# Performance work log

Hardware: AMD Instinct MI355X
Metric: run time of the kernel (lower is better)

Reference implementation:

```python
import jax, jax.numpy as jnp
import numpy as np

H = 32        # num_attention_heads
KVH = 8       # num_key_value_heads
D = 2048      # hidden_size
HD = D // H   # head_dim = 64
GROUPS = H // KVH


def setup_inputs() -> dict:
    key = jax.random.key(0)
    k1, k2, k3, k4 = jax.random.split(key, 4)
    B, T = 2, 2048
    x = jax.random.normal(k1, (B, T, D), dtype=jnp.float32)
    wq = jax.random.normal(k2, (D, H * HD), dtype=jnp.float32) * (D ** -0.5)
    wkv = jax.random.normal(k3, (D, 2 * KVH * HD), dtype=jnp.float32) * (D ** -0.5)
    wo = jax.random.normal(k4, (H * HD, D), dtype=jnp.float32) * (D ** -0.5)
    return {"x": x, "wq": wq, "wkv": wkv, "wo": wo}


def reference(x, wq, wkv, wo):
    B, T, _ = x.shape
    scale = HD ** -0.5
    # projections
    q = (x @ wq).reshape(B, T, H, HD).transpose(0, 2, 1, 3)        # [B,H,T,hd]
    kv = x @ wkv                                                    # [B,T,2*KVH*hd]
    k, v = jnp.split(kv, 2, axis=-1)
    k = k.reshape(B, T, KVH, HD).transpose(0, 2, 1, 3)              # [B,KVH,T,hd]
    v = v.reshape(B, T, KVH, HD).transpose(0, 2, 1, 3)
    # repeat_interleave KV heads to match Q heads
    k = jnp.repeat(k, GROUPS, axis=1)                               # [B,H,T,hd]
    v = jnp.repeat(v, GROUPS, axis=1)
    scores = jnp.einsum('bhqd,bhkd->bhqk', q, k) * scale            # [B,H,T,T]
    causal = jnp.triu(jnp.ones((T, T), dtype=bool), k=1)
    scores = jnp.where(causal, -jnp.inf, scores)
    attn = jax.nn.softmax(scores, axis=-1)
    out = jnp.einsum('bhqk,bhkd->bhqd', attn, v)                    # [B,H,T,hd]
    out = out.transpose(0, 2, 1, 3).reshape(B, T, H * HD)
    return out @ wo
```

## Files before the change

kernel.cpp:

```cpp
#include <hip/hip_runtime.h>

using bf16   = __bf16;
using bf16x8 = __attribute__((ext_vector_type(8))) __bf16;
using f32x4  = __attribute__((ext_vector_type(4))) float;

#define T_SEQ 2048
#define NQKV 3072

__device__ __forceinline__ void async_cp16(const bf16* g, bf16* l) {
  __builtin_amdgcn_global_load_lds((__attribute__((address_space(1))) void*)(void*)g,
                                   (__attribute__((address_space(3))) void*)l, 16, 0, 0);
}

__global__ __launch_bounds__(256) void cvt_kernel(const float* __restrict__ in,
                                                  bf16* __restrict__ out) {
  long i = ((long)blockIdx.x * 256 + threadIdx.x) * 8;
  float4 a = *(const float4*)(in + i);
  float4 c = *(const float4*)(in + i + 4);
  bf16x8 v;
  v[0] = (bf16)a.x; v[1] = (bf16)a.y; v[2] = (bf16)a.z; v[3] = (bf16)a.w;
  v[4] = (bf16)c.x; v[5] = (bf16)c.y; v[6] = (bf16)c.z; v[7] = (bf16)c.w;
  *(bf16x8*)(out + i) = v;
}

__global__ __launch_bounds__(256) void transpose_cvt(const float* __restrict__ in,
                                                     bf16* __restrict__ out,
                                                     int R, int C) {
  __shared__ float tile[32][33];
  const int tc = blockIdx.x * 32;
  const int tr = blockIdx.y * 32;
  const int t = threadIdx.x;
  const int lr = t >> 5;
  const int lc = t & 31;
#pragma unroll
  for (int i = 0; i < 4; ++i)
    tile[lr + i * 8][lc] = in[(size_t)(tr + lr + i * 8) * C + tc + lc];
  __syncthreads();
#pragma unroll
  for (int i = 0; i < 4; ++i)
    out[(size_t)(tc + lr + i * 8) * R + tr + lc] = (bf16)tile[lc][lr + i * 8];
}

__global__ __launch_bounds__(256) void transpose_v(const bf16* __restrict__ in,
                                                   bf16* __restrict__ out) {
  __shared__ bf16 tile[32][33];
  const int c0 = blockIdx.x * 32;
  const int r0 = blockIdx.y * 32;
  const int t = threadIdx.x;
  const int lr = t >> 5;
  const int lc = t & 31;
#pragma unroll
  for (int i = 0; i < 4; ++i)
    tile[lr + i * 8][lc] = in[(size_t)(r0 + lr + i * 8) * NQKV + 2560 + c0 + lc];
  __syncthreads();
#pragma unroll
  for (int i = 0; i < 4; ++i) {
    int c = c0 + lr + i * 8;
    int r = r0 + lc;
    out[(size_t)((r >> 11) * 512 + c) * 2048 + (r & 2047)] = tile[lc][lr + i * 8];
  }
}

template <bool OUT_BF16>
__global__ __launch_bounds__(256, 3)
void gemm_kernel(const bf16* __restrict__ A, const bf16* __restrict__ Bt,
                 void* __restrict__ Cout, int Kdim, int Ndim) {
  __shared__ __attribute__((aligned(16))) bf16 As[128 * 64];
  __shared__ __attribute__((aligned(16))) bf16 Bs[128 * 64];
  const int tid  = threadIdx.x;
  const int lane = tid & 63;
  const int wave = tid >> 6;
  const int l16  = lane & 15;
  const int q4   = lane >> 4;
  const long m0 = (long)blockIdx.y * 128;
  const long n0 = (long)blockIdx.x * 128;
  const int wm = (wave >> 1) * 64;
  const int wn = (wave & 1) * 64;

  f32x4 acc[4][4] = {};

  for (int k0 = 0; k0 < Kdim; k0 += 64) {
    __syncthreads();
#pragma unroll
    for (int rr = 0; rr < 4; ++rr) {
      int ci  = rr * 256 + tid;
      int row = ci >> 3;
      int chp = ci & 7;
      int ch  = chp ^ (row & 7);
      async_cp16(A + (m0 + row) * (long)Kdim + k0 + ch * 8, &As[ci * 8]);
      async_cp16(Bt + (n0 + row) * (long)Kdim + k0 + ch * 8, &Bs[ci * 8]);
    }
    __syncthreads();
#pragma unroll
    for (int ks = 0; ks < 2; ++ks) {
      bf16x8 af[4], bfr[4];
#pragma unroll
      for (int mt = 0; mt < 4; ++mt) {
        int row = wm + mt * 16 + l16;
        int chp = (ks * 4 + q4) ^ (row & 7);
        af[mt] = *(const bf16x8*)&As[row * 64 + chp * 8];
      }
#pragma unroll
      for (int nt = 0; nt < 4; ++nt) {
        int row = wn + nt * 16 + l16;
        int chp = (ks * 4 + q4) ^ (row & 7);
        bfr[nt] = *(const bf16x8*)&Bs[row * 64 + chp * 8];
      }
#pragma unroll
      for (int mt = 0; mt < 4; ++mt)
#pragma unroll
        for (int nt = 0; nt < 4; ++nt)
          acc[mt][nt] = __builtin_amdgcn_mfma_f32_16x16x32_bf16(af[mt], bfr[nt],
                                                                acc[mt][nt], 0, 0, 0);
    }
  }
#pragma unroll
  for (int mt = 0; mt < 4; ++mt)
#pragma unroll
    for (int nt = 0; nt < 4; ++nt)
#pragma unroll
      for (int r = 0; r < 4; ++r) {
        long row = m0 + wm + mt * 16 + q4 * 4 + r;
        long col = n0 + wn + nt * 16 + l16;
        float v = acc[mt][nt][r];
        if constexpr (OUT_BF16)
          ((bf16*)Cout)[row * Ndim + col] = (bf16)v;
        else
          ((float*)Cout)[row * Ndim + col] = v;
      }
}

__global__ __launch_bounds__(256, 3)
void attn_kernel(const bf16* __restrict__ qkv, const bf16* __restrict__ vT,
                 bf16* __restrict__ outb) {
  __shared__ __attribute__((aligned(16))) bf16 Ks[64 * 72];
  __shared__ __attribute__((aligned(16))) bf16 Vs[64 * 72];
  __shared__ __attribute__((aligned(16))) bf16 Ps[4][32 * 72];

  const int tid  = threadIdx.x;
  const int lane = tid & 63;
  const int wave = tid >> 6;
  const int l16  = lane & 15;
  const int q4   = lane >> 4;

  const int bid = blockIdx.x;
  const int qt  = 15 - (bid >> 6);
  const int bh  = bid & 63;
  const int b   = bh >> 5;
  const int h   = bh & 31;
  const int kvh = h >> 2;
  const long rowbase = (long)b * T_SEQ;

  const int qrow0 = qt * 128;
  const int wq0   = qrow0 + wave * 32;
  const float cexp = 0.125f * 1.4426950408889634f;

  bf16x8 aq[2][2];
#pragma unroll
  for (int mt = 0; mt < 2; ++mt)
#pragma unroll
    for (int ks = 0; ks < 2; ++ks)
      aq[mt][ks] = *(const bf16x8*)(qkv +
          (rowbase + wq0 + mt * 16 + l16) * (long)NQKV + h * 64 + ks * 32 + q4 * 8);

  bf16x8 ones_f;
#pragma unroll
  for (int i = 0; i < 8; ++i) ones_f[i] = (l16 == 0) ? (bf16)1.0f : (bf16)0.0f;

  f32x4 o[2][4] = {};
  f32x4 o_l[2] = {};

  for (int j0 = 0; j0 < qrow0 + 128; j0 += 64) {
    __syncthreads();
    {
      int r  = tid >> 2;
      int c0 = (tid & 3) * 16;
      const bf16* srcK = qkv + (rowbase + j0 + r) * (long)NQKV + 2048 + kvh * 64 + c0;
      *(bf16x8*)&Ks[r * 72 + c0]     = *(const bf16x8*)srcK;
      *(bf16x8*)&Ks[r * 72 + c0 + 8] = *(const bf16x8*)(srcK + 8);
      const bf16* srcV = vT + ((long)b * 512 + kvh * 64 + r) * 2048 + j0 + c0;
      *(bf16x8*)&Vs[r * 72 + c0]     = *(const bf16x8*)srcV;
      *(bf16x8*)&Vs[r * 72 + c0 + 8] = *(const bf16x8*)(srcV + 8);
    }
    __syncthreads();
    if (j0 > wq0 + 31) continue;

    f32x4 s[2][4] = {};
#pragma unroll
    for (int ks = 0; ks < 2; ++ks) {
      bf16x8 bk[4];
#pragma unroll
      for (int nt = 0; nt < 4; ++nt)
        bk[nt] = *(const bf16x8*)&Ks[(nt * 16 + l16) * 72 + ks * 32 + q4 * 8];
#pragma unroll
      for (int mt = 0; mt < 2; ++mt)
#pragma unroll
        for (int nt = 0; nt < 4; ++nt)
          s[mt][nt] = __builtin_amdgcn_mfma_f32_16x16x32_bf16(aq[mt][ks], bk[nt],
                                                              s[mt][nt], 0, 0, 0);
    }

    if (j0 + 63 > wq0) {
#pragma unroll
      for (int mt = 0; mt < 2; ++mt)
#pragma unroll
        for (int nt = 0; nt < 4; ++nt)
#pragma unroll
          for (int r = 0; r < 4; ++r) {
            int rg = wq0 + mt * 16 + q4 * 4 + r;
            int cg = j0 + nt * 16 + l16;
            if (cg > rg) s[mt][nt][r] = -__builtin_inff();
          }
    }

#pragma unroll
    for (int mt = 0; mt < 2; ++mt)
#pragma unroll
      for (int nt = 0; nt < 4; ++nt)
#pragma unroll
        for (int r = 0; r < 4; ++r) {
          float pv = exp2f(s[mt][nt][r] * cexp);
          Ps[wave][(mt * 16 + q4 * 4 + r) * 72 + nt * 16 + l16] = (bf16)pv;
        }

#pragma unroll
    for (int ks = 0; ks < 2; ++ks) {
      bf16x8 ap[2], bv[4];
#pragma unroll
      for (int mt = 0; mt < 2; ++mt)
        ap[mt] = *(const bf16x8*)&Ps[wave][(mt * 16 + l16) * 72 + ks * 32 + q4 * 8];
#pragma unroll
      for (int dt = 0; dt < 4; ++dt)
        bv[dt] = *(const bf16x8*)&Vs[(dt * 16 + l16) * 72 + ks * 32 + q4 * 8];
#pragma unroll
      for (int mt = 0; mt < 2; ++mt) {
#pragma unroll
        for (int dt = 0; dt < 4; ++dt)
          o[mt][dt] = __builtin_amdgcn_mfma_f32_16x16x32_bf16(ap[mt], bv[dt],
                                                              o[mt][dt], 0, 0, 0);
        o_l[mt] = __builtin_amdgcn_mfma_f32_16x16x32_bf16(ap[mt], ones_f,
                                                          o_l[mt], 0, 0, 0);
      }
    }
  }

#pragma unroll
  for (int mt = 0; mt < 2; ++mt) {
    float inv[4];
#pragma unroll
    for (int r = 0; r < 4; ++r) {
      float lsum = __shfl(o_l[mt][r], lane & 48);
      inv[r] = 1.0f / lsum;
    }
#pragma unroll
    for (int dt = 0; dt < 4; ++dt)
#pragma unroll
      for (int r = 0; r < 4; ++r) {
        long row = rowbase + qrow0 + wave * 32 + mt * 16 + q4 * 4 + r;
        int col = h * 64 + dt * 16 + l16;
        outb[row * 2048 + col] = (bf16)(o[mt][dt][r] * inv[r]);
      }
  }
}

extern "C" void kernel_launch(void* const* d_in, const int* in_sizes, int n_in,
                              void* d_out, int out_size, void* d_ws, size_t ws_size,
                              hipStream_t stream) {
  const float* x   = (const float*)d_in[0];
  const float* wq  = (const float*)d_in[1];
  const float* wkv = (const float*)d_in[2];
  const float* wo  = (const float*)d_in[3];
  float* out = (float*)d_out;
  char* ws = (char*)d_ws;

  bf16* xbf  = (bf16*)(ws + 0);
  bf16* w1   = (bf16*)(ws + 16777216);
  bf16* qkv  = (bf16*)(ws + 29360128);
  bf16* attn = xbf;
  bf16* vT   = w1;

  const size_t need_parallel = 54525952u + 8388608u;
  bf16* woT;
  bool woT_early;
  if (ws_size >= need_parallel) {
    woT = (bf16*)(ws + 54525952);
    woT_early = true;
  } else {
    woT = qkv;
    woT_early = false;
  }

  cvt_kernel<<<4096, 256, 0, stream>>>(x, xbf);
  transpose_cvt<<<dim3(64, 64), 256, 0, stream>>>(wq, w1, 2048, 2048);
  transpose_cvt<<<dim3(32, 64), 256, 0, stream>>>(wkv, w1 + 2048L * 2048, 2048, 1024);
  if (woT_early)
    transpose_cvt<<<dim3(64, 64), 256, 0, stream>>>(wo, woT, 2048, 2048);

  gemm_kernel<true><<<dim3(24, 32), 256, 0, stream>>>(xbf, w1, (void*)qkv, 2048, 3072);

  transpose_v<<<dim3(16, 128), 256, 0, stream>>>(qkv, vT);

  attn_kernel<<<1024, 256, 0, stream>>>(qkv, vT, attn);

  if (!woT_early)
    transpose_cvt<<<dim3(64, 64), 256, 0, stream>>>(wo, woT, 2048, 2048);

  gemm_kernel<false><<<dim3(16, 32), 256, 0, stream>>>(attn, woT, (void*)out, 2048, 2048);
}
```

Before: 279.4 us.

## Use 64-row query tiles with paired causal tiles per block for load balance

The attention kernel now processes 64-row query tiles (16 rows per wave) and each block handles two tiles, qt and 31-qt, so every block does roughly the same amount of causal work. This halves per-wave accumulator registers and the P staging buffer, and raises the occupancy hint from 3 to 4 blocks per CU. In exchange, each K/V tile loaded into LDS feeds only 16 query rows per wave, so reuse of the staged data per load drops.

```diff
diff --git a/kernel.cpp b/kernel.cpp
--- a/kernel.cpp
+++ b/kernel.cpp
@@ -130,12 +130,12 @@
       }
 }
 
-__global__ __launch_bounds__(256, 3)
+__global__ __launch_bounds__(256, 4)
 void attn_kernel(const bf16* __restrict__ qkv, const bf16* __restrict__ vT,
                  bf16* __restrict__ outb) {
   __shared__ __attribute__((aligned(16))) bf16 Ks[64 * 72];
   __shared__ __attribute__((aligned(16))) bf16 Vs[64 * 72];
-  __shared__ __attribute__((aligned(16))) bf16 Ps[4][32 * 72];
+  __shared__ __attribute__((aligned(16))) bf16 Ps[4][16 * 72];
 
   const int tid  = threadIdx.x;
   const int lane = tid & 63;
@@ -144,121 +144,107 @@
   const int q4   = lane >> 4;
 
   const int bid = blockIdx.x;
-  const int qt  = 15 - (bid >> 6);
+  const int pairi = bid >> 6;
   const int bh  = bid & 63;
   const int b   = bh >> 5;
   const int h   = bh & 31;
   const int kvh = h >> 2;
   const long rowbase = (long)b * T_SEQ;
-
-  const int qrow0 = qt * 128;
-  const int wq0   = qrow0 + wave * 32;
   const float cexp = 0.125f * 1.4426950408889634f;
 
-  bf16x8 aq[2][2];
-#pragma unroll
-  for (int mt = 0; mt < 2; ++mt)
+  bf16x8 ones_f;
+#pragma unroll
+  for (int i = 0; i < 8; ++i) ones_f[i] = (l16 == 0) ? (bf16)1.0f : (bf16)0.0f;
+
+#pragma unroll
+  for (int ph = 0; ph < 2; ++ph) {
+    const int qt    = ph ? (31 - pairi) : pairi;
+    const int qrow0 = qt * 64;
+    const int wq0   = qrow0 + wave * 16;
+
+    bf16x8 aq[2];
 #pragma unroll
     for (int ks = 0; ks < 2; ++ks)
-      aq[mt][ks] = *(const bf16x8*)(qkv +
-          (rowbase + wq0 + mt * 16 + l16) * (long)NQKV + h * 64 + ks * 32 + q4 * 8);
-
-  bf16x8 ones_f;
-#pragma unroll
-  for (int i = 0; i < 8; ++i) ones_f[i] = (l16 == 0) ? (bf16)1.0f : (bf16)0.0f;
-
-  f32x4 o[2][4] = {};
-  f32x4 o_l[2] = {};
-
-  for (int j0 = 0; j0 < qrow0 + 128; j0 += 64) {
-    __syncthreads();
-    {
-      int r  = tid >> 2;
-      int c0 = (tid & 3) * 16;
-      const bf16* srcK = qkv + (rowbase + j0 + r) * (long)NQKV + 2048 + kvh * 64 + c0;
-      *(bf16x8*)&Ks[r * 72 + c0]     = *(const bf16x8*)srcK;
-      *(bf16x8*)&Ks[r * 72 + c0 + 8] = *(const bf16x8*)(srcK + 8);
-      const bf16* srcV = vT + ((long)b * 512 + kvh * 64 + r) * 2048 + j0 + c0;
-      *(bf16x8*)&Vs[r * 72 + c0]     = *(const bf16x8*)srcV;
-      *(bf16x8*)&Vs[r * 72 + c0 + 8] = *(const bf16x8*)(srcV + 8);
-    }
-    __syncthreads();
-    if (j0 > wq0 + 31) continue;
-
-    f32x4 s[2][4] = {};
-#pragma unroll
-    for (int ks = 0; ks < 2; ++ks) {
-      bf16x8 bk[4];
+      aq[ks] = *(const bf16x8*)(qkv +
+          (rowbase + wq0 + l16) * (long)NQKV + h * 64 + ks * 32 + q4 * 8);
+
+    f32x4 o[4] = {};
+    f32x4 o_l = {};
+
+    for (int j0 = 0; j0 <= qrow0; j0 += 64) {
+      __syncthreads();
+      {
+        int r  = tid >> 2;
+        int c0 = (tid & 3) * 16;
+        const bf16* srcK = qkv + (rowbase + j0 + r) * (long)NQKV + 2048 + kvh * 64 + c0;
+        *(bf16x8*)&Ks[r * 72 + c0]     = *(const bf16x8*)srcK;
+        *(bf16x8*)&Ks[r * 72 + c0 + 8] = *(const bf16x8*)(srcK + 8);
+        const bf16* srcV = vT + ((long)b * 512 + kvh * 64 + r) * 2048 + j0 + c0;
+        *(bf16x8*)&Vs[r * 72 + c0]     = *(const bf16x8*)srcV;
+        *(bf16x8*)&Vs[r * 72 + c0 + 8] = *(const bf16x8*)(srcV + 8);
+      }
+      __syncthreads();
+      if (j0 > wq0 + 15) continue;
+
+      f32x4 s[4] = {};
+#pragma unroll
+      for (int ks = 0; ks < 2; ++ks) {
+        bf16x8 bk[4];
+#pragma unroll
+        for (int nt = 0; nt < 4; ++nt)
+          bk[nt] = *(const bf16x8*)&Ks[(nt * 16 + l16) * 72 + ks * 32 + q4 * 8];
+#pragma unroll
+        for (int nt = 0; nt < 4; ++nt)
+          s[nt] = __builtin_amdgcn_mfma_f32_16x16x32_bf16(aq[ks], bk[nt],
+                                                          s[nt], 0, 0, 0);
+      }
+
+      if (j0 + 63 > wq0) {
+#pragma unroll
+        for (int nt = 0; nt < 4; ++nt)
+#pragma unroll
+          for (int r = 0; r < 4; ++r) {
+            int rg = wq0 + q4 * 4 + r;
+            int cg = j0 + nt * 16 + l16;
+            if (cg > rg) s[nt][r] = -__builtin_inff();
+          }
+      }
+
 #pragma unroll
       for (int nt = 0; nt < 4; ++nt)
-        bk[nt] = *(const bf16x8*)&Ks[(nt * 16 + l16) * 72 + ks * 32 + q4 * 8];
-#pragma unroll
-      for (int mt = 0; mt < 2; ++mt)
-#pragma unroll
-        for (int nt = 0; nt < 4; ++nt)
-          s[mt][nt] = __builtin_amdgcn_mfma_f32_16x16x32_bf16(aq[mt][ks], bk[nt],
-                                                              s[mt][nt], 0, 0, 0);
-    }
-
-    if (j0 + 63 > wq0) {
-#pragma unroll
-      for (int mt = 0; mt < 2; ++mt)
-#pragma unroll
-        for (int nt = 0; nt < 4; ++nt)
-#pragma unroll
-          for (int r = 0; r < 4; ++r) {
-            int rg = wq0 + mt * 16 + q4 * 4 + r;
-            int cg = j0 + nt * 16 + l16;
-            if (cg > rg) s[mt][nt][r] = -__builtin_inff();
-          }
-    }
-
-#pragma unroll
-    for (int mt = 0; mt < 2; ++mt)
-#pragma unroll
-      for (int nt = 0; nt < 4; ++nt)
 #pragma unroll
         for (int r = 0; r < 4; ++r) {
-          float pv = exp2f(s[mt][nt][r] * cexp);
-          Ps[wave][(mt * 16 + q4 * 4 + r) * 72 + nt * 16 + l16] = (bf16)pv;
+          float pv = exp2f(s[nt][r] * cexp);
+          Ps[wave][(q4 * 4 + r) * 72 + nt * 16 + l16] = (bf16)pv;
         }
 
 #pragma unroll
-    for (int ks = 0; ks < 2; ++ks) {
-      bf16x8 ap[2], bv[4];
-#pragma unroll
-      for (int mt = 0; mt < 2; ++mt)
-        ap[mt] = *(const bf16x8*)&Ps[wave][(mt * 16 + l16) * 72 + ks * 32 + q4 * 8];
-#pragma unroll
-      for (int dt = 0; dt < 4; ++dt)
-        bv[dt] = *(const bf16x8*)&Vs[(dt * 16 + l16) * 72 + ks * 32 + q4 * 8];
-#pragma unroll
-      for (int mt = 0; mt < 2; ++mt) {
+      for (int ks = 0; ks < 2; ++ks) {
+        bf16x8 ap = *(const bf16x8*)&Ps[wave][l16 * 72 + ks * 32 + q4 * 8];
+        bf16x8 bv[4];
 #pragma unroll
         for (int dt = 0; dt < 4; ++dt)
-          o[mt][dt] = __builtin_amdgcn_mfma_f32_16x16x32_bf16(ap[mt], bv[dt],
-                                                              o[mt][dt], 0, 0, 0);
-        o_l[mt] = __builtin_amdgcn_mfma_f32_16x16x32_bf16(ap[mt], ones_f,
-                                                          o_l[mt], 0, 0, 0);
-      }
-    }
-  }
-
-#pragma unroll
-  for (int mt = 0; mt < 2; ++mt) {
+          bv[dt] = *(const bf16x8*)&Vs[(dt * 16 + l16) * 72 + ks * 32 + q4 * 8];
+#pragma unroll
+        for (int dt = 0; dt < 4; ++dt)
+          o[dt] = __builtin_amdgcn_mfma_f32_16x16x32_bf16(ap, bv[dt], o[dt], 0, 0, 0);
+        o_l = __builtin_amdgcn_mfma_f32_16x16x32_bf16(ap, ones_f, o_l, 0, 0, 0);
+      }
+    }
+
     float inv[4];
 #pragma unroll
     for (int r = 0; r < 4; ++r) {
-      float lsum = __shfl(o_l[mt][r], lane & 48);
+      float lsum = __shfl(o_l[r], lane & 48);
       inv[r] = 1.0f / lsum;
     }
 #pragma unroll
     for (int dt = 0; dt < 4; ++dt)
 #pragma unroll
       for (int r = 0; r < 4; ++r) {
-        long row = rowbase + qrow0 + wave * 32 + mt * 16 + q4 * 4 + r;
+        long row = rowbase + wq0 + q4 * 4 + r;
         int col = h * 64 + dt * 16 + l16;
-        outb[row * 2048 + col] = (bf16)(o[mt][dt][r] * inv[r]);
+        outb[row * 2048 + col] = (bf16)(o[dt][r] * inv[r]);
       }
   }
 }
```

New measurement: 286.2 us. 1.02x slower.

## Pair causal q-tiles per attention block and merge prep kernels into one launch

Applied to the files above, without the earlier changes.

The attention kernel now runs 512 blocks of 512 threads, and each block handles two complementary causal query tiles (qt and 15-qt). The two tiles share the K/V loads staged in LDS, which balances work across blocks and halves the K/V global traffic per pair. The input conversion and weight transposes are also fused into a single prep launch to cut launch overhead. The cost is more LDS per block for the larger P buffer and idle waves in the short-tile group during the later K/V iterations.

```diff
diff --git a/kernel.cpp b/kernel.cpp
--- a/kernel.cpp
+++ b/kernel.cpp
@@ -12,33 +12,56 @@
                                    (__attribute__((address_space(3))) void*)l, 16, 0, 0);
 }
 
-__global__ __launch_bounds__(256) void cvt_kernel(const float* __restrict__ in,
-                                                  bf16* __restrict__ out) {
-  long i = ((long)blockIdx.x * 256 + threadIdx.x) * 8;
-  float4 a = *(const float4*)(in + i);
-  float4 c = *(const float4*)(in + i + 4);
-  bf16x8 v;
-  v[0] = (bf16)a.x; v[1] = (bf16)a.y; v[2] = (bf16)a.z; v[3] = (bf16)a.w;
-  v[4] = (bf16)c.x; v[5] = (bf16)c.y; v[6] = (bf16)c.z; v[7] = (bf16)c.w;
-  *(bf16x8*)(out + i) = v;
+__device__ __forceinline__ void transpose_body(const float* __restrict__ in,
+                                               bf16* __restrict__ out,
+                                               int bx, int by, int R, int C) {
+  __shared__ float tile[32][33];
+  const int tc = bx * 32;
+  const int tr = by * 32;
+  const int t = threadIdx.x;
+  const int lr = t >> 5;
+  const int lc = t & 31;
+#pragma unroll
+  for (int i = 0; i < 4; ++i)
+    tile[lr + i * 8][lc] = in[(size_t)(tr + lr + i * 8) * C + tc + lc];
+  __syncthreads();
+#pragma unroll
+  for (int i = 0; i < 4; ++i)
+    out[(size_t)(tc + lr + i * 8) * R + tr + lc] = (bf16)tile[lc][lr + i * 8];
+}
+
+__global__ __launch_bounds__(256) void prep_kernel(const float* __restrict__ x,
+                                                   const float* __restrict__ wq,
+                                                   const float* __restrict__ wkv,
+                                                   const float* __restrict__ wo,
+                                                   bf16* __restrict__ xbf,
+                                                   bf16* __restrict__ w1,
+                                                   bf16* __restrict__ woT) {
+  const int i = blockIdx.x;
+  if (i < 4096) {
+    long e = ((long)i * 256 + threadIdx.x) * 8;
+    float4 a = *(const float4*)(x + e);
+    float4 c = *(const float4*)(x + e + 4);
+    bf16x8 v;
+    v[0] = (bf16)a.x; v[1] = (bf16)a.y; v[2] = (bf16)a.z; v[3] = (bf16)a.w;
+    v[4] = (bf16)c.x; v[5] = (bf16)c.y; v[6] = (bf16)c.z; v[7] = (bf16)c.w;
+    *(bf16x8*)(xbf + e) = v;
+  } else if (i < 8192) {
+    int idx = i - 4096;
+    transpose_body(wq, w1, idx & 63, idx >> 6, 2048, 2048);
+  } else if (i < 10240) {
+    int idx = i - 8192;
+    transpose_body(wkv, w1 + 2048L * 2048, idx & 31, idx >> 5, 2048, 1024);
+  } else {
+    int idx = i - 10240;
+    transpose_body(wo, woT, idx & 63, idx >> 6, 2048, 2048);
+  }
 }
 
 __global__ __launch_bounds__(256) void transpose_cvt(const float* __restrict__ in,
                                                      bf16* __restrict__ out,
                                                      int R, int C) {
-  __shared__ float tile[32][33];
-  const int tc = blockIdx.x * 32;
-  const int tr = blockIdx.y * 32;
-  const int t = threadIdx.x;
-  const int lr = t >> 5;
-  const int lc = t & 31;
-#pragma unroll
-  for (int i = 0; i < 4; ++i)
-    tile[lr + i * 8][lc] = in[(size_t)(tr + lr + i * 8) * C + tc + lc];
-  __syncthreads();
-#pragma unroll
-  for (int i = 0; i < 4; ++i)
-    out[(size_t)(tc + lr + i * 8) * R + tr + lc] = (bf16)tile[lc][lr + i * 8];
+  transpose_body(in, out, blockIdx.x, blockIdx.y, R, C);
 }
 
 __global__ __launch_bounds__(256) void transpose_v(const bf16* __restrict__ in,
@@ -130,29 +153,32 @@
       }
 }
 
-__global__ __launch_bounds__(256, 3)
+__global__ __launch_bounds__(512, 4)
 void attn_kernel(const bf16* __restrict__ qkv, const bf16* __restrict__ vT,
                  bf16* __restrict__ outb) {
   __shared__ __attribute__((aligned(16))) bf16 Ks[64 * 72];
   __shared__ __attribute__((aligned(16))) bf16 Vs[64 * 72];
-  __shared__ __attribute__((aligned(16))) bf16 Ps[4][32 * 72];
+  __shared__ __attribute__((aligned(16))) bf16 Ps[8][32 * 72];
 
   const int tid  = threadIdx.x;
   const int lane = tid & 63;
   const int wave = tid >> 6;
+  const int grp  = wave >> 2;
+  const int wavein = wave & 3;
   const int l16  = lane & 15;
   const int q4   = lane >> 4;
 
   const int bid = blockIdx.x;
-  const int qt  = 15 - (bid >> 6);
+  const int pairi = bid >> 6;
   const int bh  = bid & 63;
   const int b   = bh >> 5;
   const int h   = bh & 31;
   const int kvh = h >> 2;
   const long rowbase = (long)b * T_SEQ;
 
+  const int qt    = grp ? (15 - pairi) : pairi;
   const int qrow0 = qt * 128;
-  const int wq0   = qrow0 + wave * 32;
+  const int wq0   = qrow0 + wavein * 32;
   const float cexp = 0.125f * 1.4426950408889634f;
 
   bf16x8 aq[2][2];
@@ -170,17 +196,16 @@
   f32x4 o[2][4] = {};
   f32x4 o_l[2] = {};
 
-  for (int j0 = 0; j0 < qrow0 + 128; j0 += 64) {
+  const int jend = (16 - pairi) * 128;
+  for (int j0 = 0; j0 < jend; j0 += 64) {
     __syncthreads();
     {
-      int r  = tid >> 2;
-      int c0 = (tid & 3) * 16;
-      const bf16* srcK = qkv + (rowbase + j0 + r) * (long)NQKV + 2048 + kvh * 64 + c0;
-      *(bf16x8*)&Ks[r * 72 + c0]     = *(const bf16x8*)srcK;
-      *(bf16x8*)&Ks[r * 72 + c0 + 8] = *(const bf16x8*)(srcK + 8);
-      const bf16* srcV = vT + ((long)b * 512 + kvh * 64 + r) * 2048 + j0 + c0;
-      *(bf16x8*)&Vs[r * 72 + c0]     = *(const bf16x8*)srcV;
-      *(bf16x8*)&Vs[r * 72 + c0 + 8] = *(const bf16x8*)(srcV + 8);
+      int r  = tid >> 3;
+      int c0 = (tid & 7) * 8;
+      *(bf16x8*)&Ks[r * 72 + c0] =
+          *(const bf16x8*)(qkv + (rowbase + j0 + r) * (long)NQKV + 2048 + kvh * 64 + c0);
+      *(bf16x8*)&Vs[r * 72 + c0] =
+          *(const bf16x8*)(vT + ((long)b * 512 + kvh * 64 + r) * 2048 + j0 + c0);
     }
     __syncthreads();
     if (j0 > wq0 + 31) continue;
@@ -256,7 +281,7 @@
     for (int dt = 0; dt < 4; ++dt)
 #pragma unroll
       for (int r = 0; r < 4; ++r) {
-        long row = rowbase + qrow0 + wave * 32 + mt * 16 + q4 * 4 + r;
+        long row = rowbase + wq0 + mt * 16 + q4 * 4 + r;
         int col = h * 64 + dt * 16 + l16;
         outb[row * 2048 + col] = (bf16)(o[mt][dt][r] * inv[r]);
       }
@@ -290,17 +315,14 @@
     woT_early = false;
   }
 
-  cvt_kernel<<<4096, 256, 0, stream>>>(x, xbf);
-  transpose_cvt<<<dim3(64, 64), 256, 0, stream>>>(wq, w1, 2048, 2048);
-  transpose_cvt<<<dim3(32, 64), 256, 0, stream>>>(wkv, w1 + 2048L * 2048, 2048, 1024);
-  if (woT_early)
-    transpose_cvt<<<dim3(64, 64), 256, 0, stream>>>(wo, woT, 2048, 2048);
+  prep_kernel<<<woT_early ? 14336 : 10240, 256, 0, stream>>>(x, wq, wkv, wo,
+                                                             xbf, w1, woT);
 
   gemm_kernel<true><<<dim3(24, 32), 256, 0, stream>>>(xbf, w1, (void*)qkv, 2048, 3072);
 
   transpose_v<<<dim3(16, 128), 256, 0, stream>>>(qkv, vT);
 
-  attn_kernel<<<1024, 256, 0, stream>>>(qkv, vT, attn);
+  attn_kernel<<<512, 512, 0, stream>>>(qkv, vT, attn);
 
   if (!woT_early)
     transpose_cvt<<<dim3(64, 64), 256, 0, stream>>>(wo, woT, 2048, 2048);
```

Result: slower. 323.8 us (+15.9%).

## Produce V transposed directly from a batched GEMM and rebalance attention tile order

Applied to the files above, without the earlier changes.

V is now computed as W_v^T·x^T in a separate batched GEMM launch, with blockIdx.z indexing the batch. That writes V^T straight into its buffer and removes both the transpose_v kernel and the V columns of the QKV output. The QKV GEMM shrinks to 2560 output columns, and the workspace offsets shift to match. Attention query tiles are also launched in a snake order so causal-mask work is spread more evenly across waves of blocks. The extra V GEMM launch has only 128 blocks, so it may underfill the GPU.

```diff
diff --git a/kernel.cpp b/kernel.cpp
--- a/kernel.cpp
+++ b/kernel.cpp
@@ -5,7 +5,7 @@
 using f32x4  = __attribute__((ext_vector_type(4))) float;
 
 #define T_SEQ 2048
-#define NQKV 3072
+#define QKS 2560
 
 __device__ __forceinline__ void async_cp16(const bf16* g, bf16* l) {
   __builtin_amdgcn_global_load_lds((__attribute__((address_space(1))) void*)(void*)g,
@@ -41,30 +41,11 @@
     out[(size_t)(tc + lr + i * 8) * R + tr + lc] = (bf16)tile[lc][lr + i * 8];
 }
 
-__global__ __launch_bounds__(256) void transpose_v(const bf16* __restrict__ in,
-                                                   bf16* __restrict__ out) {
-  __shared__ bf16 tile[32][33];
-  const int c0 = blockIdx.x * 32;
-  const int r0 = blockIdx.y * 32;
-  const int t = threadIdx.x;
-  const int lr = t >> 5;
-  const int lc = t & 31;
-#pragma unroll
-  for (int i = 0; i < 4; ++i)
-    tile[lr + i * 8][lc] = in[(size_t)(r0 + lr + i * 8) * NQKV + 2560 + c0 + lc];
-  __syncthreads();
-#pragma unroll
-  for (int i = 0; i < 4; ++i) {
-    int c = c0 + lr + i * 8;
-    int r = r0 + lc;
-    out[(size_t)((r >> 11) * 512 + c) * 2048 + (r & 2047)] = tile[lc][lr + i * 8];
-  }
-}
-
 template <bool OUT_BF16>
 __global__ __launch_bounds__(256, 3)
 void gemm_kernel(const bf16* __restrict__ A, const bf16* __restrict__ Bt,
-                 void* __restrict__ Cout, int Kdim, int Ndim) {
+                 void* __restrict__ Cout, int Kdim, int Ndim,
+                 long zBt, long zC) {
   __shared__ __attribute__((aligned(16))) bf16 As[128 * 64];
   __shared__ __attribute__((aligned(16))) bf16 Bs[128 * 64];
   const int tid  = threadIdx.x;
@@ -76,6 +57,7 @@
   const long n0 = (long)blockIdx.x * 128;
   const int wm = (wave >> 1) * 64;
   const int wn = (wave & 1) * 64;
+  Bt += (long)blockIdx.z * zBt;
 
   f32x4 acc[4][4] = {};
 
@@ -124,9 +106,9 @@
         long col = n0 + wn + nt * 16 + l16;
         float v = acc[mt][nt][r];
         if constexpr (OUT_BF16)
-          ((bf16*)Cout)[row * Ndim + col] = (bf16)v;
+          ((bf16*)Cout)[(long)blockIdx.z * zC + row * Ndim + col] = (bf16)v;
         else
-          ((float*)Cout)[row * Ndim + col] = v;
+          ((float*)Cout)[(long)blockIdx.z * zC + row * Ndim + col] = v;
       }
 }
 
@@ -144,7 +126,8 @@
   const int q4   = lane >> 4;
 
   const int bid = blockIdx.x;
-  const int qt  = 15 - (bid >> 6);
+  static const int qmap[16] = {15,14,13,12, 8,9,10,11, 7,6,5,4, 0,1,2,3};
+  const int qt  = qmap[bid >> 6];
   const int bh  = bid & 63;
   const int b   = bh >> 5;
   const int h   = bh & 31;
@@ -161,7 +144,7 @@
 #pragma unroll
     for (int ks = 0; ks < 2; ++ks)
       aq[mt][ks] = *(const bf16x8*)(qkv +
-          (rowbase + wq0 + mt * 16 + l16) * (long)NQKV + h * 64 + ks * 32 + q4 * 8);
+          (rowbase + wq0 + mt * 16 + l16) * (long)QKS + h * 64 + ks * 32 + q4 * 8);
 
   bf16x8 ones_f;
 #pragma unroll
@@ -175,7 +158,7 @@
     {
       int r  = tid >> 2;
       int c0 = (tid & 3) * 16;
-      const bf16* srcK = qkv + (rowbase + j0 + r) * (long)NQKV + 2048 + kvh * 64 + c0;
+      const bf16* srcK = qkv + (rowbase + j0 + r) * (long)QKS + 2048 + kvh * 64 + c0;
       *(bf16x8*)&Ks[r * 72 + c0]     = *(const bf16x8*)srcK;
       *(bf16x8*)&Ks[r * 72 + c0 + 8] = *(const bf16x8*)(srcK + 8);
       const bf16* srcV = vT + ((long)b * 512 + kvh * 64 + r) * 2048 + j0 + c0;
@@ -256,7 +239,7 @@
     for (int dt = 0; dt < 4; ++dt)
 #pragma unroll
       for (int r = 0; r < 4; ++r) {
-        long row = rowbase + qrow0 + wave * 32 + mt * 16 + q4 * 4 + r;
+        long row = rowbase + wq0 + mt * 16 + q4 * 4 + r;
         int col = h * 64 + dt * 16 + l16;
         outb[row * 2048 + col] = (bf16)(o[mt][dt][r] * inv[r]);
       }
@@ -279,11 +262,11 @@
   bf16* attn = xbf;
   bf16* vT   = w1;
 
-  const size_t need_parallel = 54525952u + 8388608u;
+  const size_t need_parallel = 50331648u + 8388608u;
   bf16* woT;
   bool woT_early;
   if (ws_size >= need_parallel) {
-    woT = (bf16*)(ws + 54525952);
+    woT = (bf16*)(ws + 50331648);
     woT_early = true;
   } else {
     woT = qkv;
@@ -296,14 +279,18 @@
   if (woT_early)
     transpose_cvt<<<dim3(64, 64), 256, 0, stream>>>(wo, woT, 2048, 2048);
 
-  gemm_kernel<true><<<dim3(24, 32), 256, 0, stream>>>(xbf, w1, (void*)qkv, 2048, 3072);
-
-  transpose_v<<<dim3(16, 128), 256, 0, stream>>>(qkv, vT);
+  gemm_kernel<true><<<dim3(20, 32), 256, 0, stream>>>(xbf, w1, (void*)qkv,
+                                                      2048, 2560, 0, 0);
+
+  gemm_kernel<true><<<dim3(16, 4, 2), 256, 0, stream>>>(w1 + 2560L * 2048, xbf,
+                                                        (void*)vT, 2048, 2048,
+                                                        2048L * 2048, 512L * 2048);
 
   attn_kernel<<<1024, 256, 0, stream>>>(qkv, vT, attn);
 
   if (!woT_early)
     transpose_cvt<<<dim3(64, 64), 256, 0, stream>>>(wo, woT, 2048, 2048);
 
-  gemm_kernel<false><<<dim3(16, 32), 256, 0, stream>>>(attn, woT, (void*)out, 2048, 2048);
-}
+  gemm_kernel<false><<<dim3(16, 32), 256, 0, stream>>>(attn, woT, (void*)out,
+                                                       2048, 2048, 0, 0);
+}
```

New measurement: 305.3 us. 1.09x slower.
